# Optimization experiments

Measured on AMD Instinct MI355X. Metric: run time of the kernel, lower is better.

Reference implementation:

```python
import jax, jax.numpy as jnp
import numpy as np

D_MODEL = 256
HIDDEN = 128
TAU = 0.5
ATTN_SCALE = D_MODEL ** -0.5


def setup_inputs() -> dict:
    key = jax.random.key(0)
    ks = jax.random.split(key, 10)
    B, P, K, N = 16, 87, 4, 32768
    s = lambda fan_in: (1.0 / np.sqrt(fan_in)).astype(np.float32)
    return {
        "human_queries": jax.random.normal(ks[0], (B, P, D_MODEL), jnp.float32),
        "object_queries": jax.random.normal(ks[1], (B, K, D_MODEL), jnp.float32),
        "object_feats": jax.random.normal(ks[2], (B, N, D_MODEL), jnp.float32),
        "object_xyz": jax.random.normal(ks[3], (B, N, 3), jnp.float32),
        # human_head: Linear(d_model->hidden), ReLU, Dropout(eval=identity), Linear(hidden->1)
        "W1": jax.random.uniform(ks[4], (D_MODEL, HIDDEN), jnp.float32, -s(D_MODEL), s(D_MODEL)),
        "b1": jnp.zeros((HIDDEN,), jnp.float32),
        "W2": jax.random.uniform(ks[5], (HIDDEN, 1), jnp.float32, -s(HIDDEN), s(HIDDEN)),
        "b2": jnp.zeros((1,), jnp.float32),
        # object_query_proj: Linear(d_model->d_model)
        "Wq": jax.random.uniform(ks[6], (D_MODEL, D_MODEL), jnp.float32, -s(D_MODEL), s(D_MODEL)),
        "bq": jnp.zeros((D_MODEL,), jnp.float32),
    }


def reference(human_queries, object_queries, object_feats, object_xyz,
              W1, b1, W2, b2, Wq, bq):
    # Human contact head: small MLP -> sigmoid. Dropout is eval-mode identity.
    h = jax.nn.relu(human_queries @ W1 + b1)            # (B, 87, hidden)
    human_logits = (h @ W2 + b2)[..., 0]                # (B, 87)
    human_probs = jax.nn.sigmoid(human_logits)
    # Temperature-scaled cross-attention pooling over N points.
    q = object_queries @ Wq + bq                        # (B, K, d)
    logits = jnp.einsum("bkd,bnd->bkn", q, object_feats) * ATTN_SCALE
    weights = jax.nn.softmax(logits / TAU, axis=-1)     # (B, K, N)
    object_coords = jnp.einsum("bkn,bnc->bkc", weights, object_xyz)  # (B, K, 3)
    return (human_probs, human_logits, object_coords)
```

## Files before the change

kernel.cpp:

```cpp
#include <hip/hip_runtime.h>
#include <hip/hip_bf16.h>

typedef float f4 __attribute__((ext_vector_type(4)));

constexpr int B   = 16;
constexpr int P   = 87;
constexpr int K   = 4;
constexpr int N   = 32768;
constexpr int D   = 256;
constexpr int HID = 128;
constexpr int CH  = 128;
constexpr int CHN = N / CH;
constexpr float SCL = 0.125f;

constexpr int HB  = (B * P) / 4;

__device__ __forceinline__ f4 ntload(const float* p) {
    return __builtin_nontemporal_load((const f4*)p);
}

__global__ __launch_bounds__(256) void qproj(const float* __restrict__ oq,
                                             const float* __restrict__ Wq,
                                             const float* __restrict__ bq,
                                             float* __restrict__ q) {
    const int row = blockIdx.x;
    const int j   = threadIdx.x;
    const float* x = oq + (size_t)row * D;
    float a0 = bq[j], a1 = 0.f, a2 = 0.f, a3 = 0.f;
#pragma unroll 4
    for (int i = 0; i < D; i += 4) {
        a0 = fmaf(x[i + 0], Wq[(size_t)(i + 0) * D + j], a0);
        a1 = fmaf(x[i + 1], Wq[(size_t)(i + 1) * D + j], a1);
        a2 = fmaf(x[i + 2], Wq[(size_t)(i + 2) * D + j], a2);
        a3 = fmaf(x[i + 3], Wq[(size_t)(i + 3) * D + j], a3);
    }
    q[(size_t)row * D + j] = (a0 + a1) + (a2 + a3);
}

__global__ __launch_bounds__(256) void fused_main(const float* __restrict__ feats,
                                                  const float* __restrict__ xyz,
                                                  const float* __restrict__ q,
                                                  const float* __restrict__ hq,
                                                  const float* __restrict__ W1,
                                                  const float* __restrict__ b1,
                                                  const float* __restrict__ W2,
                                                  const float* __restrict__ b2,
                                                  float* __restrict__ part,
                                                  float* __restrict__ out) {
    __shared__ float sxyz[CHN * 3];
    __shared__ float red[4][K * 4];
    __shared__ float sred[2][2][2];

    const int bid = blockIdx.x;
    const int tid = threadIdx.x;

    if (bid < HB) {
        const int j    = tid & (HID - 1);
        const int rp   = tid >> 7;
        const int row0 = bid * 4 + rp * 2;

        const float* x0 = hq + (size_t)row0 * D;
        const float* x1 = x0 + D;
        float acc0 = b1[j];
        float acc1 = acc0;
#pragma unroll 4
        for (int i = 0; i < D; ++i) {
            const float wv = W1[(size_t)i * HID + j];
            acc0 = fmaf(x0[i], wv, acc0);
            acc1 = fmaf(x1[i], wv, acc1);
        }
        const float w2 = W2[j];
        float v0 = fmaxf(acc0, 0.f) * w2;
        float v1 = fmaxf(acc1, 0.f) * w2;
#pragma unroll
        for (int off = 32; off; off >>= 1) {
            v0 += __shfl_xor(v0, off);
            v1 += __shfl_xor(v1, off);
        }
        const int lane = tid & 63;
        const int wh   = (tid >> 6) & 1;
        if (lane == 0) { sred[rp][wh][0] = v0; sred[rp][wh][1] = v1; }
        __syncthreads();
        if (tid < 2) {
            const float bb = b2[0];
            const float l0 = sred[tid][0][0] + sred[tid][1][0] + bb;
            const float l1 = sred[tid][0][1] + sred[tid][1][1] + bb;
            const int r = bid * 4 + tid * 2;
            out[B * P + r + 0] = l0;
            out[B * P + r + 1] = l1;
            out[r + 0] = 1.f / (1.f + __expf(-l0));
            out[r + 1] = 1.f / (1.f + __expf(-l1));
        }
        return;
    }

    const int abid = bid - HB;
    const int b    = abid >> 7;
    const int ch   = abid & (CH - 1);
    const int lane = tid & 63;
    const int w    = tid >> 6;
    const int sg   = lane >> 4;
    const int m    = lane & 15;

    const float* xsrc = xyz + ((size_t)b * N + (size_t)ch * CHN) * 3;
    for (int i = tid; i < CHN * 3; i += 256) sxyz[i] = xsrc[i];

    f4 qv[K][4];
#pragma unroll
    for (int k = 0; k < K; ++k)
#pragma unroll
        for (int j = 0; j < 4; ++j)
            qv[k][j] = *(const f4*)(q + (size_t)(b * K + k) * D + j * 64 + m * 4);

    __syncthreads();

    const float* fbase = feats + ((size_t)b * N + (size_t)ch * CHN) * D;

    float s_[K] = {0.f, 0.f, 0.f, 0.f};
    float ax[K] = {0.f, 0.f, 0.f, 0.f};
    float ay[K] = {0.f, 0.f, 0.f, 0.f};
    float az[K] = {0.f, 0.f, 0.f, 0.f};

    constexpr int NG = CHN / 4;

    f4 f0, f1, f2, f3;
    {
        const float* rp = fbase + (size_t)(w * 4 + sg) * D + m * 4;
        f0 = ntload(rp + 0);
        f1 = ntload(rp + 64);
        f2 = ntload(rp + 128);
        f3 = ntload(rp + 192);
    }

    for (int g = w; g < NG; g += 4) {
        const f4 c0 = f0, c1 = f1, c2 = f2, c3 = f3;
        const int gn = g + 4;
        if (gn < NG) {
            const float* rp = fbase + (size_t)(gn * 4 + sg) * D + m * 4;
            f0 = ntload(rp + 0);
            f1 = ntload(rp + 64);
            f2 = ntload(rp + 128);
            f3 = ntload(rp + 192);
        }
        const int r = g * 4 + sg;

        float d[K];
#pragma unroll
        for (int k = 0; k < K; ++k) {
            float t0 = c0.x * qv[k][0].x;
            t0 = fmaf(c0.y, qv[k][0].y, t0);
            t0 = fmaf(c0.z, qv[k][0].z, t0);
            t0 = fmaf(c0.w, qv[k][0].w, t0);
            float t1 = c1.x * qv[k][1].x;
            t1 = fmaf(c1.y, qv[k][1].y, t1);
            t1 = fmaf(c1.z, qv[k][1].z, t1);
            t1 = fmaf(c1.w, qv[k][1].w, t1);
            t0 = fmaf(c2.x, qv[k][2].x, t0);
            t0 = fmaf(c2.y, qv[k][2].y, t0);
            t0 = fmaf(c2.z, qv[k][2].z, t0);
            t0 = fmaf(c2.w, qv[k][2].w, t0);
            t1 = fmaf(c3.x, qv[k][3].x, t1);
            t1 = fmaf(c3.y, qv[k][3].y, t1);
            t1 = fmaf(c3.z, qv[k][3].z, t1);
            t1 = fmaf(c3.w, qv[k][3].w, t1);
            d[k] = t0 + t1;
        }
#pragma unroll
        for (int k = 0; k < K; ++k) {
            float v = d[k];
            v += __shfl_xor(v, 8);
            v += __shfl_xor(v, 4);
            v += __shfl_xor(v, 2);
            v += __shfl_xor(v, 1);
            d[k] = v;
        }

        const float x = sxyz[r * 3 + 0];
        const float y = sxyz[r * 3 + 1];
        const float z = sxyz[r * 3 + 2];
#pragma unroll
        for (int k = 0; k < K; ++k) {
            const float e = __expf(d[k] * SCL);
            s_[k] += e;
            ax[k] = fmaf(e, x, ax[k]);
            ay[k] = fmaf(e, y, ay[k]);
            az[k] = fmaf(e, z, az[k]);
        }
    }

#pragma unroll
    for (int k = 0; k < K; ++k) {
        float v;
        v = s_[k]; v += __shfl_xor(v, 16); v += __shfl_xor(v, 32); s_[k] = v;
        v = ax[k]; v += __shfl_xor(v, 16); v += __shfl_xor(v, 32); ax[k] = v;
        v = ay[k]; v += __shfl_xor(v, 16); v += __shfl_xor(v, 32); ay[k] = v;
        v = az[k]; v += __shfl_xor(v, 16); v += __shfl_xor(v, 32); az[k] = v;
    }
    if (lane == 0) {
#pragma unroll
        for (int k = 0; k < K; ++k) {
            red[w][k * 4 + 0] = s_[k];
            red[w][k * 4 + 1] = ax[k];
            red[w][k * 4 + 2] = ay[k];
            red[w][k * 4 + 3] = az[k];
        }
    }
    __syncthreads();
    if (tid < K * 4) {
        const float v = red[0][tid] + red[1][tid] + red[2][tid] + red[3][tid];
        part[((size_t)b * CH + ch) * (K * 4) + tid] = v;
    }
}

__global__ __launch_bounds__(192) void finalize(const float* __restrict__ part,
                                                float* __restrict__ out) {
    const int t = threadIdx.x;
    if (t >= B * K * 3) return;
    const int c  = t % 3;
    const int bk = t / 3;
    const int k  = bk % K;
    const int b  = bk / K;
    float S = 0.f, V = 0.f;
    for (int ch = 0; ch < CH; ++ch) {
        const float* p = part + (((size_t)b * CH + ch) * K + k) * 4;
        S += p[0];
        V += p[1 + c];
    }
    out[2 * B * P + (b * K + k) * 3 + c] = V / S;
}

extern "C" void kernel_launch(void* const* d_in, const int* in_sizes, int n_in,
                              void* d_out, int out_size, void* d_ws, size_t ws_size,
                              hipStream_t stream) {
    const float* hq    = (const float*)d_in[0];
    const float* oq    = (const float*)d_in[1];
    const float* feats = (const float*)d_in[2];
    const float* xyz   = (const float*)d_in[3];
    const float* W1    = (const float*)d_in[4];
    const float* b1    = (const float*)d_in[5];
    const float* W2    = (const float*)d_in[6];
    const float* b2    = (const float*)d_in[7];
    const float* Wq    = (const float*)d_in[8];
    const float* bq    = (const float*)d_in[9];
    float* out = (float*)d_out;

    float* q    = (float*)d_ws;
    float* part = q + (size_t)B * K * D;

    qproj<<<B * K, 256, 0, stream>>>(oq, Wq, bq, q);
    fused_main<<<HB + B * CH, 256, 0, stream>>>(feats, xyz, q, hq, W1, b1, W2, b2,
                                                part, out);
    finalize<<<1, 192, 0, stream>>>(part, out);
}
```

Measured before the change: 109.4 us.

## Fuse query projection into main kernel and parallelize finalize reduction

Removes the separate qproj launch: each attention block recomputes the 4x256 query projection for its batch into shared memory, overlapping with the first feature prefetch. The finalize kernel now uses one block per batch with vectorized loads and wave shuffles instead of a single block of serial loops. This saves a launch and the serial reduction, but every one of the 2048 attention blocks redundantly reads the 256 KB Wq matrix and does a 256x256x4 matvec before streaming features.

```diff
diff --git a/kernel.cpp b/kernel.cpp
--- a/kernel.cpp
+++ b/kernel.cpp
@@ -19,27 +19,11 @@
     return __builtin_nontemporal_load((const f4*)p);
 }
 
-__global__ __launch_bounds__(256) void qproj(const float* __restrict__ oq,
-                                             const float* __restrict__ Wq,
-                                             const float* __restrict__ bq,
-                                             float* __restrict__ q) {
-    const int row = blockIdx.x;
-    const int j   = threadIdx.x;
-    const float* x = oq + (size_t)row * D;
-    float a0 = bq[j], a1 = 0.f, a2 = 0.f, a3 = 0.f;
-#pragma unroll 4
-    for (int i = 0; i < D; i += 4) {
-        a0 = fmaf(x[i + 0], Wq[(size_t)(i + 0) * D + j], a0);
-        a1 = fmaf(x[i + 1], Wq[(size_t)(i + 1) * D + j], a1);
-        a2 = fmaf(x[i + 2], Wq[(size_t)(i + 2) * D + j], a2);
-        a3 = fmaf(x[i + 3], Wq[(size_t)(i + 3) * D + j], a3);
-    }
-    q[(size_t)row * D + j] = (a0 + a1) + (a2 + a3);
-}
-
 __global__ __launch_bounds__(256) void fused_main(const float* __restrict__ feats,
                                                   const float* __restrict__ xyz,
-                                                  const float* __restrict__ q,
+                                                  const float* __restrict__ oq,
+                                                  const float* __restrict__ Wq,
+                                                  const float* __restrict__ bq,
                                                   const float* __restrict__ hq,
                                                   const float* __restrict__ W1,
                                                   const float* __restrict__ b1,
@@ -48,6 +32,7 @@
                                                   float* __restrict__ part,
                                                   float* __restrict__ out) {
     __shared__ float sxyz[CHN * 3];
+    __shared__ float sq[K][D];
     __shared__ float red[4][K * 4];
     __shared__ float sred[2][2][2];
 
@@ -102,25 +87,7 @@
     const int sg   = lane >> 4;
     const int m    = lane & 15;
 
-    const float* xsrc = xyz + ((size_t)b * N + (size_t)ch * CHN) * 3;
-    for (int i = tid; i < CHN * 3; i += 256) sxyz[i] = xsrc[i];
-
-    f4 qv[K][4];
-#pragma unroll
-    for (int k = 0; k < K; ++k)
-#pragma unroll
-        for (int j = 0; j < 4; ++j)
-            qv[k][j] = *(const f4*)(q + (size_t)(b * K + k) * D + j * 64 + m * 4);
-
-    __syncthreads();
-
     const float* fbase = feats + ((size_t)b * N + (size_t)ch * CHN) * D;
-
-    float s_[K] = {0.f, 0.f, 0.f, 0.f};
-    float ax[K] = {0.f, 0.f, 0.f, 0.f};
-    float ay[K] = {0.f, 0.f, 0.f, 0.f};
-    float az[K] = {0.f, 0.f, 0.f, 0.f};
-
     constexpr int NG = CHN / 4;
 
     f4 f0, f1, f2, f3;
@@ -131,6 +98,41 @@
         f2 = ntload(rp + 128);
         f3 = ntload(rp + 192);
     }
+
+    const float* xsrc = xyz + ((size_t)b * N + (size_t)ch * CHN) * 3;
+    for (int i = tid; i < CHN * 3; i += 256) sxyz[i] = xsrc[i];
+
+    {
+        const int j = tid;
+        const float* oqb = oq + (size_t)b * K * D;
+        const float bv = bq[j];
+        float qa0 = bv, qa1 = bv, qa2 = bv, qa3 = bv;
+#pragma unroll 4
+        for (int i = 0; i < D; ++i) {
+            const float wv = Wq[(size_t)i * D + j];
+            qa0 = fmaf(oqb[0 * D + i], wv, qa0);
+            qa1 = fmaf(oqb[1 * D + i], wv, qa1);
+            qa2 = fmaf(oqb[2 * D + i], wv, qa2);
+            qa3 = fmaf(oqb[3 * D + i], wv, qa3);
+        }
+        sq[0][j] = qa0;
+        sq[1][j] = qa1;
+        sq[2][j] = qa2;
+        sq[3][j] = qa3;
+    }
+    __syncthreads();
+
+    f4 qv[K][4];
+#pragma unroll
+    for (int k = 0; k < K; ++k)
+#pragma unroll
+        for (int j = 0; j < 4; ++j)
+            qv[k][j] = *(const f4*)(&sq[k][j * 64 + m * 4]);
+
+    float s_[K] = {0.f, 0.f, 0.f, 0.f};
+    float ax[K] = {0.f, 0.f, 0.f, 0.f};
+    float ay[K] = {0.f, 0.f, 0.f, 0.f};
+    float az[K] = {0.f, 0.f, 0.f, 0.f};
 
     for (int g = w; g < NG; g += 4) {
         const f4 c0 = f0, c1 = f1, c2 = f2, c3 = f3;
@@ -212,21 +214,31 @@
     }
 }
 
-__global__ __launch_bounds__(192) void finalize(const float* __restrict__ part,
+__global__ __launch_bounds__(256) void finalize(const float* __restrict__ part,
                                                 float* __restrict__ out) {
-    const int t = threadIdx.x;
-    if (t >= B * K * 3) return;
-    const int c  = t % 3;
-    const int bk = t / 3;
-    const int k  = bk % K;
-    const int b  = bk / K;
-    float S = 0.f, V = 0.f;
-    for (int ch = 0; ch < CH; ++ch) {
-        const float* p = part + (((size_t)b * CH + ch) * K + k) * 4;
-        S += p[0];
-        V += p[1 + c];
-    }
-    out[2 * B * P + (b * K + k) * 3 + c] = V / S;
+    const int b = blockIdx.x;
+    const int w = threadIdx.x >> 6;
+    const int l = threadIdx.x & 63;
+
+    const float* pb = part + (size_t)b * CH * (K * 4) + w * 4;
+    f4 v = *(const f4*)(pb + (size_t)l * (K * 4));
+    f4 u = *(const f4*)(pb + (size_t)(l + 64) * (K * 4));
+    v.x += u.x; v.y += u.y; v.z += u.z; v.w += u.w;
+
+#pragma unroll
+    for (int off = 32; off; off >>= 1) {
+        v.x += __shfl_xor(v.x, off);
+        v.y += __shfl_xor(v.y, off);
+        v.z += __shfl_xor(v.z, off);
+        v.w += __shfl_xor(v.w, off);
+    }
+    if (l == 0) {
+        const float inv = 1.f / v.x;
+        float* o = out + 2 * B * P + (b * K + w) * 3;
+        o[0] = v.y * inv;
+        o[1] = v.z * inv;
+        o[2] = v.w * inv;
+    }
 }
 
 extern "C" void kernel_launch(void* const* d_in, const int* in_sizes, int n_in,
@@ -244,11 +256,9 @@
     const float* bq    = (const float*)d_in[9];
     float* out = (float*)d_out;
 
-    float* q    = (float*)d_ws;
-    float* part = q + (size_t)B * K * D;
-
-    qproj<<<B * K, 256, 0, stream>>>(oq, Wq, bq, q);
-    fused_main<<<HB + B * CH, 256, 0, stream>>>(feats, xyz, q, hq, W1, b1, W2, b2,
-                                                part, out);
-    finalize<<<1, 192, 0, stream>>>(part, out);
-}
+    float* part = (float*)d_ws;
+
+    fused_main<<<HB + B * CH, 256, 0, stream>>>(feats, xyz, oq, Wq, bq,
+                                                hq, W1, b1, W2, b2, part, out);
+    finalize<<<B, 256, 0, stream>>>(part, out);
+}
```

Result: slower. 123.7 us (+13.1%).

## Reorder blocks, issue feature prefetch early, parallelize finalize reduction

Applied to the files above, without the earlier changes.

Attention blocks now come first in the grid and the human-MLP blocks are placed last, so the bandwidth-heavy work starts immediately. The first feature loads are issued before the xyz staging and query loads, letting that latency overlap with shared-memory setup. The finalize kernel switches from one block running serial per-thread loops over 128 chunks to 16 blocks that use vector loads and wave shuffles. These changes target launch tail and latency overhead; the main kernel stays limited by streaming feats from memory.

```diff
diff --git a/kernel.cpp b/kernel.cpp
--- a/kernel.cpp
+++ b/kernel.cpp
@@ -13,6 +13,7 @@
 constexpr int CHN = N / CH;
 constexpr float SCL = 0.125f;
 
+constexpr int AB  = B * CH;
 constexpr int HB  = (B * P) / 4;
 
 __device__ __forceinline__ f4 ntload(const float* p) {
@@ -54,10 +55,11 @@
     const int bid = blockIdx.x;
     const int tid = threadIdx.x;
 
-    if (bid < HB) {
+    if (bid >= AB) {
+        const int hbid = bid - AB;
         const int j    = tid & (HID - 1);
         const int rp   = tid >> 7;
-        const int row0 = bid * 4 + rp * 2;
+        const int row0 = hbid * 4 + rp * 2;
 
         const float* x0 = hq + (size_t)row0 * D;
         const float* x1 = x0 + D;
@@ -85,7 +87,7 @@
             const float bb = b2[0];
             const float l0 = sred[tid][0][0] + sred[tid][1][0] + bb;
             const float l1 = sred[tid][0][1] + sred[tid][1][1] + bb;
-            const int r = bid * 4 + tid * 2;
+            const int r = hbid * 4 + tid * 2;
             out[B * P + r + 0] = l0;
             out[B * P + r + 1] = l1;
             out[r + 0] = 1.f / (1.f + __expf(-l0));
@@ -94,33 +96,14 @@
         return;
     }
 
-    const int abid = bid - HB;
-    const int b    = abid >> 7;
-    const int ch   = abid & (CH - 1);
+    const int b    = bid >> 7;
+    const int ch   = bid & (CH - 1);
     const int lane = tid & 63;
     const int w    = tid >> 6;
     const int sg   = lane >> 4;
     const int m    = lane & 15;
 
-    const float* xsrc = xyz + ((size_t)b * N + (size_t)ch * CHN) * 3;
-    for (int i = tid; i < CHN * 3; i += 256) sxyz[i] = xsrc[i];
-
-    f4 qv[K][4];
-#pragma unroll
-    for (int k = 0; k < K; ++k)
-#pragma unroll
-        for (int j = 0; j < 4; ++j)
-            qv[k][j] = *(const f4*)(q + (size_t)(b * K + k) * D + j * 64 + m * 4);
-
-    __syncthreads();
-
     const float* fbase = feats + ((size_t)b * N + (size_t)ch * CHN) * D;
-
-    float s_[K] = {0.f, 0.f, 0.f, 0.f};
-    float ax[K] = {0.f, 0.f, 0.f, 0.f};
-    float ay[K] = {0.f, 0.f, 0.f, 0.f};
-    float az[K] = {0.f, 0.f, 0.f, 0.f};
-
     constexpr int NG = CHN / 4;
 
     f4 f0, f1, f2, f3;
@@ -131,6 +114,23 @@
         f2 = ntload(rp + 128);
         f3 = ntload(rp + 192);
     }
+
+    const float* xsrc = xyz + ((size_t)b * N + (size_t)ch * CHN) * 3;
+    for (int i = tid; i < CHN * 3; i += 256) sxyz[i] = xsrc[i];
+
+    f4 qv[K][4];
+#pragma unroll
+    for (int k = 0; k < K; ++k)
+#pragma unroll
+        for (int j = 0; j < 4; ++j)
+            qv[k][j] = *(const f4*)(q + (size_t)(b * K + k) * D + j * 64 + m * 4);
+
+    __syncthreads();
+
+    float s_[K] = {0.f, 0.f, 0.f, 0.f};
+    float ax[K] = {0.f, 0.f, 0.f, 0.f};
+    float ay[K] = {0.f, 0.f, 0.f, 0.f};
+    float az[K] = {0.f, 0.f, 0.f, 0.f};
 
     for (int g = w; g < NG; g += 4) {
         const f4 c0 = f0, c1 = f1, c2 = f2, c3 = f3;
@@ -212,21 +212,31 @@
     }
 }
 
-__global__ __launch_bounds__(192) void finalize(const float* __restrict__ part,
+__global__ __launch_bounds__(256) void finalize(const float* __restrict__ part,
                                                 float* __restrict__ out) {
-    const int t = threadIdx.x;
-    if (t >= B * K * 3) return;
-    const int c  = t % 3;
-    const int bk = t / 3;
-    const int k  = bk % K;
-    const int b  = bk / K;
-    float S = 0.f, V = 0.f;
-    for (int ch = 0; ch < CH; ++ch) {
-        const float* p = part + (((size_t)b * CH + ch) * K + k) * 4;
-        S += p[0];
-        V += p[1 + c];
-    }
-    out[2 * B * P + (b * K + k) * 3 + c] = V / S;
+    const int b = blockIdx.x;
+    const int w = threadIdx.x >> 6;
+    const int l = threadIdx.x & 63;
+
+    const float* pb = part + (size_t)b * CH * (K * 4) + w * 4;
+    f4 v = *(const f4*)(pb + (size_t)l * (K * 4));
+    f4 u = *(const f4*)(pb + (size_t)(l + 64) * (K * 4));
+    v.x += u.x; v.y += u.y; v.z += u.z; v.w += u.w;
+
+#pragma unroll
+    for (int off = 32; off; off >>= 1) {
+        v.x += __shfl_xor(v.x, off);
+        v.y += __shfl_xor(v.y, off);
+        v.z += __shfl_xor(v.z, off);
+        v.w += __shfl_xor(v.w, off);
+    }
+    if (l == 0) {
+        const float inv = 1.f / v.x;
+        float* o = out + 2 * B * P + (b * K + w) * 3;
+        o[0] = v.y * inv;
+        o[1] = v.z * inv;
+        o[2] = v.w * inv;
+    }
 }
 
 extern "C" void kernel_launch(void* const* d_in, const int* in_sizes, int n_in,
@@ -248,7 +258,7 @@
     float* part = q + (size_t)B * K * D;
 
     qproj<<<B * K, 256, 0, stream>>>(oq, Wq, bq, q);
-    fused_main<<<HB + B * CH, 256, 0, stream>>>(feats, xyz, q, hq, W1, b1, W2, b2,
-                                                part, out);
-    finalize<<<1, 192, 0, stream>>>(part, out);
-}
+    fused_main<<<AB + HB, 256, 0, stream>>>(feats, xyz, q, hq, W1, b1, W2, b2,
+                                            part, out);
+    finalize<<<B, 256, 0, stream>>>(part, out);
+}
```

Result: faster. 104.1 us (-4.8%).
